# Kernel optimization log

Hardware: AMD Instinct MI355X
Metric: run time of the kernel (lower is better)

## Reference

```python
import jax, jax.numpy as jnp
import numpy as np

N = 8192   # num_nodes
H = 128    # hidden_dim
B = 100    # batch of events
K = 5      # num_neg_samples
TD_MAX = 10000.0
TIME_SD = jnp.array([50.0, 7.0, 15.0, 15.0])  # time_sd from forward; time_mean = 0


def setup_inputs() -> dict:
    key = jax.random.key(0)
    ks = jax.random.split(key, 16)
    p = 32.0 / N  # avg degree ~32
    A = (jax.random.uniform(ks[0], (N, N)) < p).astype(jnp.float32)
    # S init: S[v,u] = 1/D[v] for neighbors u (row-normalized A)
    S = A / (A.sum(axis=1, keepdims=True) + 1e-7)
    z0 = jax.random.normal(ks[1], (N, H)) * 0.1
    u = jax.random.randint(ks[2], (B,), 0, N)
    v = jax.random.randint(ks[3], (B,), 0, N)
    event_types = jax.random.randint(ks[4], (B,), 0, 2)
    neg_idx = jax.random.randint(ks[5], (B, 2 * K), 0, N)
    time_diff = jax.random.normal(ks[6], (B, 2, 4))
    t_bar = jax.random.uniform(ks[7], (B, N)) * 1000.0
    t = 1000.0 + 10.0 * jnp.arange(B, dtype=jnp.float32)

    def lin(k, o, i):
        k1, k2 = jax.random.split(k)
        lim = 1.0 / np.sqrt(i)
        return (jax.random.uniform(k1, (o, i), minval=-lim, maxval=lim),
                jax.random.uniform(k2, (o,), minval=-lim, maxval=lim))

    om0_w, om0_b = lin(ks[8], 1, 2 * H)
    om1_w, om1_b = lin(ks[9], 1, 2 * H)
    Wh_w, Wh_b = lin(ks[10], H, H)
    Ws_w, Ws_b = lin(ks[11], H, H)
    Wr_w, Wr_b = lin(ks[12], H, H)
    Wt_w, Wt_b = lin(ks[13], H, 4)
    return dict(u=u, v=v, event_types=event_types, neg_idx=neg_idx,
                time_diff=time_diff, t_bar=t_bar, t=t, z0=z0, A=A, S=S,
                w_t=0.5 * jnp.ones(2), alpha=0.5 * jnp.ones(2), psi=0.5 * jnp.ones(2),
                om0_w=om0_w, om0_b=om0_b, om1_w=om1_w, om1_b=om1_b,
                Wh_w=Wh_w, Wh_b=Wh_b, Ws_w=Ws_w, Ws_b=Ws_b,
                Wr_w=Wr_w, Wr_b=Wr_b, Wt_w=Wt_w, Wt_b=Wt_b)


def _forward(u, v, event_types, neg_idx, time_diff, t_bar, t, z0, A, S,
             w_t, alpha, psi, om0_w, om0_b, om1_w, om1_b,
             Wh_w, Wh_b, Ws_w, Ws_b, Wr_w, Wr_b, Wt_w, Wt_b):
    td_norm = time_diff / TIME_SD  # (td - 0) / sd

    def hawkes(zu, zv, et, td):
        # lambda = psi * log(1 + exp(g/psi)) + alpha * exp(-w_t * td/td_max)
        zc = jnp.concatenate([zu, zv], axis=-1)
        g0 = jnp.einsum('...d,d->...', zc, om0_w[0]) + om0_b[0]
        g1 = jnp.einsum('...d,d->...', zc, om1_w[0]) + om1_b[0]
        g = jnp.where(et == 0, g0, g1)
        ps, al, wt = psi[et], alpha[et], w_t[et]
        gp = jnp.clip(g / (ps + 1e-7), -75.0, 75.0)
        return ps * jnp.log1p(jnp.exp(gp)) + al * jnp.exp(-wt * (td / TD_MAX))

    ar = jnp.arange(N)

    def step(z, ev):
        u_it, v_it, et, td2, tb, t_it, neg = ev
        z_u, z_v = z[u_it], z[v_it]
        Wh_all = z @ Wh_w.T + Wh_b  # [N,H]

        def struct(node):
            # structural attention over node's neighbors (masked, not dense loop)
            mask = A[node] > 0
            q = jnp.exp(S[node]) * mask
            q = q / (q.sum() + 1e-7)
            hsig = jax.nn.sigmoid(q[:, None] * Wh_all)
            hmax = jnp.where(mask[:, None], hsig, -jnp.inf).max(axis=0)
            return jnp.where(jnp.any(mask), hmax, 0.0)

        # update of u uses struct info from v's neighborhood, and vice versa
        hs = jnp.stack([struct(v_it), struct(u_it)])  # [2,H]
        h = (hs @ Ws_w.T + Ws_b) + (jnp.stack([z_u, z_v]) @ Wr_w.T + Wr_b) + (td2 @ Wt_w.T + Wt_b)
        z_upd = jax.nn.sigmoid(h)
        z_new = z.at[u_it].set(z_upd[0]).at[v_it].set(z_upd[1])

        # negative pairs: (u, v_neg_k) then (u_neg_k, v), using z_prev
        v_neg, u_neg = neg[:K], neg[K:]
        zu_neg = jnp.concatenate([jnp.broadcast_to(z_u, (K, H)), z[u_neg]], 0)
        zv_neg = jnp.concatenate([z[v_neg], jnp.broadcast_to(z_v, (K, H))], 0)
        lt_u = jnp.concatenate([jnp.full((K,), tb[u_it]), tb[u_neg]])
        lt_v = jnp.concatenate([tb[v_neg], jnp.full((K,), tb[v_it])])
        ts_neg = t_it - jnp.maximum(lt_u, lt_v)
        ts_pos = t_it - jnp.maximum(tb[u_it], tb[v_it])

        # all-node intensity prediction (Lambda_dict path, detached in torch)
        zd = jax.lax.stop_gradient(z)
        zu_all = jnp.concatenate([jnp.broadcast_to(jax.lax.stop_gradient(z_u), (N, H)),
                                  jnp.broadcast_to(jax.lax.stop_gradient(z_v), (N, H))], 0)
        zv_all = jnp.concatenate([zd, zd], 0)
        last_t = jnp.maximum(
            jnp.concatenate([jnp.full((N,), tb[u_it]), jnp.full((N,), tb[v_it])]),
            jnp.concatenate([tb, tb]))
        lam_all = hawkes(zu_all, zv_all, jnp.full((2 * N,), et),
                         jax.lax.stop_gradient(t_it - last_t))
        m = ((ar != u_it) & (ar != v_it)).astype(lam_all.dtype)
        lam_sum = jax.lax.stop_gradient(jnp.sum(lam_all * jnp.concatenate([m, m])))

        return z_new, (z_u, z_v, zu_neg, zv_neg, ts_pos, ts_neg, lam_sum)

    _, (zu_p, zv_p, zun, zvn, ts_p, ts_n, lam_sums) = jax.lax.scan(
        step, z0, (u, v, event_types, td_norm, t_bar, t, neg_idx))

    lam_pos = hawkes(zu_p, zv_p, event_types, ts_p)            # [B]
    lam_neg = hawkes(zun, zvn, event_types[:, None], ts_n)      # [B,2K]
    return jnp.concatenate([lam_pos[:, None], lam_neg, lam_sums[:, None]], axis=1)  # [B, 2K+2]


def reference(u, v, event_types, neg_idx, time_diff, t_bar, t, z0, A, S,
              w_t, alpha, psi, om0_w, om0_b, om1_w, om1_b,
              Wh_w, Wh_b, Ws_w, Ws_b, Wr_w, Wr_b, Wt_w, Wt_b):
    return _forward(u, v, event_types, neg_idx, time_diff, t_bar, t, z0, A, S,
                    w_t, alpha, psi, om0_w, om0_b, om1_w, om1_b,
                    Wh_w, Wh_b, Ws_w, Ws_b, Wr_w, Wr_b, Wt_w, Wt_b)
```

## Files before the change

kernel.cpp:

```cpp
#include <hip/hip_runtime.h>
#include <math.h>

#define N 8192
#define H 128
#define BB 100
#define KK 5
#define MAXN 256
#define TD_MAXF 10000.0f

#define OFF_WHALLV ((size_t)N * H)
#define OFF_ZVER (OFF_WHALLV + 2 * BB * H)

__global__ __launch_bounds__(256) void prep_all_kernel(
    const float* __restrict__ Wh, const float* __restrict__ Ws,
    const float* __restrict__ Wr, const float* __restrict__ om0,
    const float* __restrict__ om1, const float* __restrict__ z0,
    float* __restrict__ WhT, float* __restrict__ WsT, float* __restrict__ WrT,
    float* __restrict__ omP, unsigned* __restrict__ flags,
    float* __restrict__ dvec0) {
  const int B0 = H * H, B1 = 2 * H * H, B2 = 3 * H * H;
  const int B3 = B2 + 2 * H, B4 = B2 + 4 * H, B5 = B4 + 4 * BB + 4;
  int idx = blockIdx.x * 256 + threadIdx.x;
  if (idx < B0) {
    int d = idx >> 7, k = idx & (H - 1);
    WhT[k * H + d] = Wh[d * H + k];
  } else if (idx < B1) {
    int e = idx - B0;
    int d = e >> 7, k = e & (H - 1);
    WsT[k * H + d] = Ws[d * H + k];
  } else if (idx < B2) {
    int e = idx - B1;
    int d = e >> 7, k = e & (H - 1);
    WrT[k * H + d] = Wr[d * H + k];
  } else if (idx < B3) {
    int e = idx - B2;
    omP[e] = om0[e];
  } else if (idx < B4) {
    int e = idx - B3;
    omP[2 * H + e] = om1[e];
  } else if (idx < B5) {
    flags[idx - B4] = 0u;
  } else if (idx < B5 + N) {
    int j = idx - B5;
    const float4* zr = (const float4*)(z0 + (size_t)j * H);
    const float4* o0 = (const float4*)om0;
    const float4* o1 = (const float4*)om1;
    float a0 = 0, b0 = 0, a1 = 0, b1 = 0;
    for (int k = 0; k < H / 4; ++k) {
      float4 zv = zr[k];
      float4 l0 = o0[k], r0 = o0[k + H / 4];
      float4 l1 = o1[k], r1 = o1[k + H / 4];
      a0 += zv.x * l0.x + zv.y * l0.y + zv.z * l0.z + zv.w * l0.w;
      b0 += zv.x * r0.x + zv.y * r0.y + zv.z * r0.z + zv.w * r0.w;
      a1 += zv.x * l1.x + zv.y * l1.y + zv.z * l1.z + zv.w * l1.w;
      b1 += zv.x * r1.x + zv.y * r1.y + zv.z * r1.z + zv.w * r1.w;
    }
    dvec0[0 * N + j] = a0;
    dvec0[1 * N + j] = b0;
    dvec0[2 * N + j] = a1;
    dvec0[3 * N + j] = b1;
  }
}

__global__ __launch_bounds__(256) void build_kernel(
    const float* __restrict__ z0, const float* __restrict__ WhT,
    const float* __restrict__ Wh_b, float* __restrict__ whall,
    const int* __restrict__ u_, const int* __restrict__ v_,
    const float* __restrict__ A, const float* __restrict__ S,
    int* __restrict__ cnt, int* __restrict__ nidx, float* __restrict__ nes,
    float* __restrict__ qsum, int* __restrict__ woff, int* __restrict__ zsrc,
    unsigned* __restrict__ need) {
  const int blk = blockIdx.x;
  const int tid = threadIdx.x;
  __shared__ float zr2[2][H];
  __shared__ int cnts[256];
  __shared__ int excl[257];
  __shared__ float ssum[256];
  __shared__ int nidxL[MAXN];
  __shared__ int uL[BB], vL[BB];

  if (blk < N / 2) {
    int r = tid >> 7, d = tid & (H - 1);
    int row = blk * 2 + r;
    zr2[r][d] = z0[(size_t)row * H + d];
    __syncthreads();
    float acc = Wh_b[d];
#pragma unroll 8
    for (int k = 0; k < H; ++k) acc += zr2[r][k] * WhT[k * H + d];
    whall[(size_t)row * H + d] = acc;
    return;
  }

  const int l = blk - N / 2;
  const int b = l >> 1, r = l & 1;
  const int node = r ? u_[b] : v_[b];
  int c = 0;
  float local = 0.0f;
  for (int it = 0; it < N / 256; ++it) {
    int j = it * 256 + tid;
    if (A[(size_t)node * N + j] > 0.0f) {
      ++c;
      local += expf(S[(size_t)node * N + j]);
    }
  }
  cnts[tid] = c;
  ssum[tid] = local;
  __syncthreads();
  if (tid == 0) {
    int s = 0;
    for (int i = 0; i < 256; ++i) { excl[i] = s; s += cnts[i]; }
    excl[256] = s;
  }
  __syncthreads();
  int p = excl[tid];
  for (int it = 0; it < N / 256; ++it) {
    int j = it * 256 + tid;
    if (A[(size_t)node * N + j] > 0.0f) {
      if (p < MAXN) {
        nidx[l * MAXN + p] = j;
        nidxL[p] = j;
        nes[l * MAXN + p] = expf(S[(size_t)node * N + j]);
      }
      ++p;
    }
  }
  if (tid < BB) {
    uL[tid] = u_[tid];
    vL[tid] = v_[tid];
  }
  __syncthreads();
  for (int s = 128; s > 0; s >>= 1) {
    if (tid < s) ssum[tid] += ssum[tid + s];
    __syncthreads();
  }
  const int cM = min(excl[256], MAXN);
  if (tid == 0) {
    cnt[l] = cM;
    qsum[l] = ssum[0];
  }
  for (int i = tid; i < cM; i += 256) {
    int n = nidxL[i];
    int a = -1, row = 0;
    for (int s = b - 1; s >= 0; --s) {
      if (vL[s] == n) { a = s; row = 1; break; }
      if (uL[s] == n) { a = s; row = 0; break; }
    }
    int off;
    if (a < 0) {
      off = n * H;
    } else {
      off = (int)OFF_WHALLV + (2 * a + row) * H;
      atomicOr(&need[b * 4 + (a >> 5)], 1u << (a & 31));
    }
    woff[l * MAXN + i] = off;
  }
  if (r == 0 && tid >= 254) {
    int which = tid - 254;
    int nd = which ? vL[b] : uL[b];
    int a = -1, row = 0;
    for (int s = b - 1; s >= 0; --s) {
      if (vL[s] == nd) { a = s; row = 1; break; }
      if (uL[s] == nd) { a = s; row = 0; break; }
    }
    int sv = -1;
    if (a >= 0) {
      sv = 2 * a + row;
      atomicOr(&need[b * 4 + (a >> 5)], 1u << (a & 31));
    }
    zsrc[2 * b + which] = sv;
  }
}

__global__ __launch_bounds__(1024) void step_kernel(
    const int* __restrict__ u_, const int* __restrict__ v_,
    const float* __restrict__ time_diff, const float* __restrict__ z0,
    const float* __restrict__ WhT, const float* __restrict__ WsT,
    const float* __restrict__ WrT, const float* __restrict__ omP,
    const float* __restrict__ Wh_b, const float* __restrict__ Ws_b,
    const float* __restrict__ Wr_b, const float* __restrict__ Wt_w,
    const float* __restrict__ Wt_b, const float* __restrict__ wsf,
    float* __restrict__ zver, float* __restrict__ whallv,
    float* __restrict__ dlog, const float* __restrict__ qsum_,
    const int* __restrict__ cnt_, const float* __restrict__ nes_,
    const int* __restrict__ woff_, const int* __restrict__ zsrc_,
    const unsigned* __restrict__ need, unsigned* done) {
  const int b = blockIdx.x;
  const int t = threadIdx.x;
  __shared__ float scratch[8][2][H];
  __shared__ float hsS[2][H];
  __shared__ float zrowS[2][H];
  __shared__ float zupdS[2][H];
  __shared__ float td2S[2][4];
  __shared__ int uvS[2];

  const int r = t >> 9;
  const int sub = (t >> 7) & 3;
  const int d = t & (H - 1);
  const int l = 2 * b + r;
  const int c = cnt_[l];
  const float iq = 1.0f / (qsum_[l] + 1e-7f);

  float mx = -INFINITY;
  for (int i = sub; i < c; i += 4) {
    int off = woff_[l * MAXN + i];
    if (off < (int)OFF_WHALLV)
      mx = fmaxf(mx, nes_[l * MAXN + i] * iq * wsf[(size_t)off + d]);
  }
  float zpre = 0.0f;
  int zs = -1;
  if (t < 256) {
    int rr = t >> 7, dd = t & (H - 1);
    zs = zsrc_[2 * b + rr];
    if (zs < 0) {
      int nd = rr ? v_[b] : u_[b];
      zpre = z0[(size_t)nd * H + dd];
    }
  }
  if (t >= 512 && t < 520) {
    int i = t - 512;
    int cc = i & 3;
    float sd = (cc == 0) ? 50.0f : ((cc == 1) ? 7.0f : 15.0f);
    td2S[i >> 2][cc] = time_diff[b * 8 + i] / sd;
  }
  if (t == 0) {
    uvS[0] = u_[b];
    uvS[1] = v_[b];
    for (int w = 0; w < 4; ++w) {
      unsigned nw = need[b * 4 + w];
      if (!nw) continue;
      while ((__hip_atomic_load(&done[w], __ATOMIC_RELAXED,
                                __HIP_MEMORY_SCOPE_AGENT) &
              nw) != nw)
        __builtin_amdgcn_s_sleep(1);
    }
    __threadfence();
  }
  __syncthreads();

  const int ub = uvS[0], vb = uvS[1];

  for (int i = sub; i < c; i += 4) {
    int off = woff_[l * MAXN + i];
    if (off >= (int)OFF_WHALLV)
      mx = fmaxf(mx, nes_[l * MAXN + i] * iq * wsf[(size_t)off + d]);
  }
  scratch[sub][r][d] = mx;
  if (t < 256) {
    int rr = t >> 7, dd = t & (H - 1);
    float zv;
    if (zs < 0)
      zv = zpre;
    else
      zv = wsf[OFF_ZVER + (size_t)zs * H + dd];
    zrowS[rr][dd] = zv;
  }
  __syncthreads();

  if (t < 2 * H) {
    int rr = t >> 7, dd = t & (H - 1);
    float m = fmaxf(fmaxf(scratch[0][rr][dd], scratch[1][rr][dd]),
                    fmaxf(scratch[2][rr][dd], scratch[3][rr][dd]));
    hsS[rr][dd] = (c > 0 || rr != r || true)
                      ? ((cnt_[2 * b + rr] > 0)
                             ? (1.0f / (1.0f + expf(-m)))
                             : 0.0f)
                      : 0.0f;
  }
  __syncthreads();

  {
    int ks = t >> 7;
    int k0 = ks * 16;
    float a0 = 0.0f, a1 = 0.0f;
#pragma unroll 4
    for (int k = k0; k < k0 + 16; ++k) {
      float ws = WsT[k * H + d], wr = WrT[k * H + d];
      a0 += hsS[0][k] * ws + zrowS[0][k] * wr;
      a1 += hsS[1][k] * ws + zrowS[1][k] * wr;
    }
    scratch[ks][0][d] = a0;
    scratch[ks][1][d] = a1;
  }
  __syncthreads();

  if (t < 2 * H) {
    int rr = t >> 7, dd = t & (H - 1);
    float acc = Ws_b[dd] + Wr_b[dd] + Wt_b[dd];
#pragma unroll
    for (int ks = 0; ks < 8; ++ks) acc += scratch[ks][rr][dd];
    acc += td2S[rr][0] * Wt_w[dd * 4 + 0] + td2S[rr][1] * Wt_w[dd * 4 + 1] +
           td2S[rr][2] * Wt_w[dd * 4 + 2] + td2S[rr][3] * Wt_w[dd * 4 + 3];
    float zu = 1.0f / (1.0f + expf(-acc));
    zupdS[rr][dd] = zu;
    zver[(size_t)(2 * b + rr) * H + dd] = zu;
  }
  __syncthreads();

  {
    int ks = t >> 7;
    int k0 = ks * 16;
    int r0 = (ub == vb) ? 1 : 0;
    float a0 = 0.0f, a1 = 0.0f;
#pragma unroll 4
    for (int k = k0; k < k0 + 16; ++k) {
      float wh = WhT[k * H + d];
      a0 += zupdS[r0][k] * wh;
      a1 += zupdS[1][k] * wh;
    }
    scratch[ks][0][d] = a0;
    scratch[ks][1][d] = a1;
  }
  __syncthreads();

  if (t < 2 * H) {
    int rr = t >> 7, dd = t & (H - 1);
    float acc = Wh_b[dd];
#pragma unroll
    for (int ks = 0; ks < 8; ++ks) acc += scratch[ks][rr][dd];
    whallv[(size_t)(2 * b + rr) * H + dd] = acc;
  } else if (t < 768) {
    int w = (t - 256) >> 6;
    int lane = t & 63;
    int row = w >> 2;
    int which = w & 3;
    int rr = (row == 0 && ub == vb) ? 1 : row;
    int wsel = which >> 1;
    int off = (which & 1) * H;
    float val = zupdS[rr][lane] * omP[wsel * 2 * H + off + lane] +
                zupdS[rr][64 + lane] * omP[wsel * 2 * H + off + 64 + lane];
    for (int s = 32; s > 0; s >>= 1) val += __shfl_down(val, s);
    if (lane == 0) dlog[b * 8 + which * 2 + row] = val;
  }
  __syncthreads();

  if (t == 0) {
    __threadfence();
    atomicOr(&done[b >> 5], 1u << (b & 31));
  }
}

__global__ __launch_bounds__(1024) void lam_kernel(
    const int* __restrict__ u, const int* __restrict__ v,
    const int* __restrict__ etypes, const int* __restrict__ neg_,
    const float* __restrict__ t_bar, const float* __restrict__ tt,
    const float* __restrict__ w_t, const float* __restrict__ alpha,
    const float* __restrict__ psi, const float* __restrict__ om0_b,
    const float* __restrict__ om1_b, const float* __restrict__ dvec0,
    const float* __restrict__ dlog, float* __restrict__ out) {
  const int b = blockIdx.x;
  const int tid = threadIdx.x;
  __shared__ float dR[N];
  __shared__ int uS[BB], vS[BB];
  __shared__ float red[1024];
  __shared__ float suS, svS;

  const int e = etypes[b];
  const int ub = u[b], vb = v[b];
  const float ps = psi[e], al = alpha[e], wt = w_t[e];
  const float ob0 = om0_b[0], ob1 = om1_b[0];
  const float ob = e ? ob1 : ob0;
  const float tcur = tt[b];
  const float inv_ps = 1.0f / (ps + 1e-7f);
  const int whichR = 2 * e + 1;
  const int whichL = 2 * e;

  if (tid < BB) {
    uS[tid] = u[tid];
    vS[tid] = v[tid];
  }
  {
    const float4* base = (const float4*)(dvec0 + (size_t)whichR * N);
    float4* dst = (float4*)dR;
    for (int i = tid; i < N / 4; i += 1024) dst[i] = base[i];
  }
  __syncthreads();

  for (int i = tid; i < b; i += 1024) {
    int ui = uS[i], vi = vS[i];
    bool u_over = (ui == vi);
    bool v_over = false;
    for (int j = i + 1; j < b; ++j) {
      int uj = uS[j], vj = vS[j];
      u_over = u_over || (uj == ui) || (vj == ui);
      v_over = v_over || (uj == vi) || (vj == vi);
    }
    if (!u_over) dR[ui] = dlog[i * 8 + whichR * 2 + 0];
    if (!v_over) dR[vi] = dlog[i * 8 + whichR * 2 + 1];
  }

  if (tid < 13) {
    auto dpre = [&](int x, int which) -> float {
      for (int bp = b - 1; bp >= 0; --bp) {
        if (vS[bp] == x) return dlog[bp * 8 + which * 2 + 1];
        if (uS[bp] == x) return dlog[bp * 8 + which * 2 + 0];
      }
      return dvec0[(size_t)which * N + x];
    };
    if (tid < 11) {
      int li, ri;
      float ltu, ltv;
      if (tid == 0) {
        li = ub; ri = vb;
        ltu = t_bar[(size_t)b * N + ub];
        ltv = t_bar[(size_t)b * N + vb];
      } else if (tid <= 5) {
        int vn = neg_[b * (2 * KK) + (tid - 1)];
        li = ub; ri = vn;
        ltu = t_bar[(size_t)b * N + ub];
        ltv = t_bar[(size_t)b * N + vn];
      } else {
        int un = neg_[b * (2 * KK) + (tid - 1)];
        li = un; ri = vb;
        ltu = t_bar[(size_t)b * N + un];
        ltv = t_bar[(size_t)b * N + vb];
      }
      float g = dpre(li, whichL) + dpre(ri, whichR) + ob;
      float gp = fminf(fmaxf(g * inv_ps, -75.0f), 75.0f);
      float ts = tcur - fmaxf(ltu, ltv);
      out[b * 12 + tid] =
          ps * log1pf(expf(gp)) + al * expf(-wt * (ts / TD_MAXF));
    } else if (tid == 11) {
      suS = dpre(ub, whichL);
    } else {
      svS = dpre(vb, whichL);
    }
  }
  __syncthreads();

  const float su = suS, sv = svS;
  const float tb_u = t_bar[(size_t)b * N + ub];
  const float tb_v = t_bar[(size_t)b * N + vb];
  const float4* tb4 = (const float4*)(t_bar + (size_t)b * N);
  const float4* dR4 = (const float4*)dR;
  float acc = 0.0f;
  for (int j4 = tid; j4 < N / 4; j4 += 1024) {
    float4 dv = dR4[j4];
    float4 tb = tb4[j4];
    float de[4] = {dv.x, dv.y, dv.z, dv.w};
    float te[4] = {tb.x, tb.y, tb.z, tb.w};
#pragma unroll
    for (int ee = 0; ee < 4; ++ee) {
      int j = j4 * 4 + ee;
      if (j == ub || j == vb) continue;
      float dd = de[ee];
      float tbj = te[ee];
      float gu = su + dd + ob;
      float gv = sv + dd + ob;
      float gpu_ = fminf(fmaxf(gu * inv_ps, -75.0f), 75.0f);
      float gpv_ = fminf(fmaxf(gv * inv_ps, -75.0f), 75.0f);
      float spl = ps * (log1pf(expf(gpu_)) + log1pf(expf(gpv_)));
      float tdu = tcur - fmaxf(tb_u, tbj);
      float tdv = tcur - fmaxf(tb_v, tbj);
      float ex =
          al * (expf(-wt * (tdu / TD_MAXF)) + expf(-wt * (tdv / TD_MAXF)));
      acc += spl + ex;
    }
  }
  red[tid] = acc;
  __syncthreads();
  for (int s = 512; s > 0; s >>= 1) {
    if (tid < s) red[tid] += red[tid + s];
    __syncthreads();
  }
  if (tid == 0) out[b * 12 + 11] = red[0];
}

extern "C" void kernel_launch(void* const* d_in, const int* in_sizes, int n_in,
                              void* d_out, int out_size, void* d_ws,
                              size_t ws_size, hipStream_t stream) {
  const int* u = (const int*)d_in[0];
  const int* v = (const int*)d_in[1];
  const int* et = (const int*)d_in[2];
  const int* neg = (const int*)d_in[3];
  const float* time_diff = (const float*)d_in[4];
  const float* t_bar = (const float*)d_in[5];
  const float* t = (const float*)d_in[6];
  const float* z0 = (const float*)d_in[7];
  const float* A = (const float*)d_in[8];
  const float* S = (const float*)d_in[9];
  const float* w_t = (const float*)d_in[10];
  const float* alpha = (const float*)d_in[11];
  const float* psi = (const float*)d_in[12];
  const float* om0_w = (const float*)d_in[13];
  const float* om0_b = (const float*)d_in[14];
  const float* om1_w = (const float*)d_in[15];
  const float* om1_b = (const float*)d_in[16];
  const float* Wh_w = (const float*)d_in[17];
  const float* Wh_b = (const float*)d_in[18];
  const float* Ws_w = (const float*)d_in[19];
  const float* Ws_b = (const float*)d_in[20];
  const float* Wr_w = (const float*)d_in[21];
  const float* Wr_b = (const float*)d_in[22];
  const float* Wt_w = (const float*)d_in[23];
  const float* Wt_b = (const float*)d_in[24];
  float* out = (float*)d_out;

  float* wsf = (float*)d_ws;
  float* whall = wsf;
  float* whallv = wsf + OFF_WHALLV;
  float* zver = wsf + OFF_ZVER;
  float* WhT = zver + 2 * BB * H;
  float* WsT = WhT + H * H;
  float* WrT = WsT + H * H;
  float* omP = WrT + H * H;
  float* dvec0 = omP + 4 * H;
  float* dlog = dvec0 + 4 * N;
  float* qsum = dlog + 8 * BB;
  int* cnt = (int*)(qsum + 2 * BB);
  int* nidx = cnt + 2 * BB;
  float* nes = (float*)(nidx + 2 * BB * MAXN);
  int* woff = (int*)(nes + 2 * BB * MAXN);
  int* zsrc = woff + 2 * BB * MAXN;
  unsigned* need = (unsigned*)(zsrc + 2 * BB);
  unsigned* done = need + 4 * BB;

  const int PREP_ELEMS = 3 * H * H + 4 * H + 4 * BB + 4 + N;
  prep_all_kernel<<<(PREP_ELEMS + 255) / 256, 256, 0, stream>>>(
      Wh_w, Ws_w, Wr_w, om0_w, om1_w, z0, WhT, WsT, WrT, omP, need, dvec0);
  build_kernel<<<N / 2 + 2 * BB, 256, 0, stream>>>(
      z0, WhT, Wh_b, whall, u, v, A, S, cnt, nidx, nes, qsum, woff, zsrc,
      need);
  step_kernel<<<BB, 1024, 0, stream>>>(
      u, v, time_diff, z0, WhT, WsT, WrT, omP, Wh_b, Ws_b, Wr_b, Wt_w, Wt_b,
      wsf, zver, whallv, dlog, qsum, cnt, nes, woff, zsrc, need, done);
  lam_kernel<<<BB, 1024, 0, stream>>>(u, v, et, neg, t_bar, t, w_t, alpha, psi,
                                      om0_b, om1_b, dvec0, dlog, out);
}
```

Baseline: 610.3 us.

## Fuse step and lambda kernels into one launch with per-block flag waits

Merges the sequential step kernel and the lambda kernel into a single 200-block launch. The lambda blocks spin on done flags until all earlier steps have finished, so they overlap with the step chain instead of waiting for a kernel boundary. The step blocks also preload their weight columns into registers and stage the neighbour offset and weight lists in shared memory before the dependency wait, taking those loads off the serial critical path. The cost is higher register and shared-memory pressure in every block and a reliance on all 200 blocks being co-resident, since the lambda blocks busy-wait on step blocks.

```diff
diff --git a/kernel.cpp b/kernel.cpp
--- a/kernel.cpp
+++ b/kernel.cpp
@@ -171,191 +171,212 @@
   }
 }
 
-__global__ __launch_bounds__(1024) void step_kernel(
+__global__ __launch_bounds__(1024) void fused_kernel(
     const int* __restrict__ u_, const int* __restrict__ v_,
-    const float* __restrict__ time_diff, const float* __restrict__ z0,
+    const int* __restrict__ et_, const int* __restrict__ neg_,
+    const float* __restrict__ time_diff, const float* __restrict__ t_bar,
+    const float* __restrict__ tt, const float* __restrict__ z0,
     const float* __restrict__ WhT, const float* __restrict__ WsT,
     const float* __restrict__ WrT, const float* __restrict__ omP,
     const float* __restrict__ Wh_b, const float* __restrict__ Ws_b,
     const float* __restrict__ Wr_b, const float* __restrict__ Wt_w,
-    const float* __restrict__ Wt_b, const float* __restrict__ wsf,
-    float* __restrict__ zver, float* __restrict__ whallv,
-    float* __restrict__ dlog, const float* __restrict__ qsum_,
-    const int* __restrict__ cnt_, const float* __restrict__ nes_,
-    const int* __restrict__ woff_, const int* __restrict__ zsrc_,
-    const unsigned* __restrict__ need, unsigned* done) {
-  const int b = blockIdx.x;
+    const float* __restrict__ Wt_b, const float* __restrict__ w_t,
+    const float* __restrict__ alpha, const float* __restrict__ psi,
+    const float* __restrict__ om0_b, const float* __restrict__ om1_b,
+    const float* __restrict__ wsf, float* __restrict__ zver,
+    float* __restrict__ whallv, float* __restrict__ dlog,
+    const float* __restrict__ qsum_, const int* __restrict__ cnt_,
+    const float* __restrict__ nes_, const int* __restrict__ woff_,
+    const int* __restrict__ zsrc_, const float* __restrict__ dvec0,
+    const unsigned* __restrict__ need, unsigned* done,
+    float* __restrict__ out) {
+  const int blk = blockIdx.x;
   const int t = threadIdx.x;
   __shared__ float scratch[8][2][H];
   __shared__ float hsS[2][H];
   __shared__ float zrowS[2][H];
   __shared__ float zupdS[2][H];
   __shared__ float td2S[2][4];
+  __shared__ int woffS[2][MAXN];
+  __shared__ float nqS[2][MAXN];
+  __shared__ int cntS[2];
   __shared__ int uvS[2];
-
-  const int r = t >> 9;
-  const int sub = (t >> 7) & 3;
-  const int d = t & (H - 1);
-  const int l = 2 * b + r;
-  const int c = cnt_[l];
-  const float iq = 1.0f / (qsum_[l] + 1e-7f);
-
-  float mx = -INFINITY;
-  for (int i = sub; i < c; i += 4) {
-    int off = woff_[l * MAXN + i];
-    if (off < (int)OFF_WHALLV)
-      mx = fmaxf(mx, nes_[l * MAXN + i] * iq * wsf[(size_t)off + d]);
-  }
-  float zpre = 0.0f;
-  int zs = -1;
-  if (t < 256) {
-    int rr = t >> 7, dd = t & (H - 1);
-    zs = zsrc_[2 * b + rr];
-    if (zs < 0) {
-      int nd = rr ? v_[b] : u_[b];
-      zpre = z0[(size_t)nd * H + dd];
-    }
-  }
-  if (t >= 512 && t < 520) {
-    int i = t - 512;
-    int cc = i & 3;
-    float sd = (cc == 0) ? 50.0f : ((cc == 1) ? 7.0f : 15.0f);
-    td2S[i >> 2][cc] = time_diff[b * 8 + i] / sd;
-  }
-  if (t == 0) {
-    uvS[0] = u_[b];
-    uvS[1] = v_[b];
-    for (int w = 0; w < 4; ++w) {
-      unsigned nw = need[b * 4 + w];
-      if (!nw) continue;
-      while ((__hip_atomic_load(&done[w], __ATOMIC_RELAXED,
-                                __HIP_MEMORY_SCOPE_AGENT) &
-              nw) != nw)
-        __builtin_amdgcn_s_sleep(1);
-    }
-    __threadfence();
-  }
-  __syncthreads();
-
-  const int ub = uvS[0], vb = uvS[1];
-
-  for (int i = sub; i < c; i += 4) {
-    int off = woff_[l * MAXN + i];
-    if (off >= (int)OFF_WHALLV)
-      mx = fmaxf(mx, nes_[l * MAXN + i] * iq * wsf[(size_t)off + d]);
-  }
-  scratch[sub][r][d] = mx;
-  if (t < 256) {
-    int rr = t >> 7, dd = t & (H - 1);
-    float zv;
-    if (zs < 0)
-      zv = zpre;
-    else
-      zv = wsf[OFF_ZVER + (size_t)zs * H + dd];
-    zrowS[rr][dd] = zv;
-  }
-  __syncthreads();
-
-  if (t < 2 * H) {
-    int rr = t >> 7, dd = t & (H - 1);
-    float m = fmaxf(fmaxf(scratch[0][rr][dd], scratch[1][rr][dd]),
-                    fmaxf(scratch[2][rr][dd], scratch[3][rr][dd]));
-    hsS[rr][dd] = (c > 0 || rr != r || true)
-                      ? ((cnt_[2 * b + rr] > 0)
-                             ? (1.0f / (1.0f + expf(-m)))
-                             : 0.0f)
-                      : 0.0f;
-  }
-  __syncthreads();
-
-  {
-    int ks = t >> 7;
-    int k0 = ks * 16;
-    float a0 = 0.0f, a1 = 0.0f;
-#pragma unroll 4
-    for (int k = k0; k < k0 + 16; ++k) {
-      float ws = WsT[k * H + d], wr = WrT[k * H + d];
-      a0 += hsS[0][k] * ws + zrowS[0][k] * wr;
-      a1 += hsS[1][k] * ws + zrowS[1][k] * wr;
-    }
-    scratch[ks][0][d] = a0;
-    scratch[ks][1][d] = a1;
-  }
-  __syncthreads();
-
-  if (t < 2 * H) {
-    int rr = t >> 7, dd = t & (H - 1);
-    float acc = Ws_b[dd] + Wr_b[dd] + Wt_b[dd];
-#pragma unroll
-    for (int ks = 0; ks < 8; ++ks) acc += scratch[ks][rr][dd];
-    acc += td2S[rr][0] * Wt_w[dd * 4 + 0] + td2S[rr][1] * Wt_w[dd * 4 + 1] +
-           td2S[rr][2] * Wt_w[dd * 4 + 2] + td2S[rr][3] * Wt_w[dd * 4 + 3];
-    float zu = 1.0f / (1.0f + expf(-acc));
-    zupdS[rr][dd] = zu;
-    zver[(size_t)(2 * b + rr) * H + dd] = zu;
-  }
-  __syncthreads();
-
-  {
-    int ks = t >> 7;
-    int k0 = ks * 16;
-    int r0 = (ub == vb) ? 1 : 0;
-    float a0 = 0.0f, a1 = 0.0f;
-#pragma unroll 4
-    for (int k = k0; k < k0 + 16; ++k) {
-      float wh = WhT[k * H + d];
-      a0 += zupdS[r0][k] * wh;
-      a1 += zupdS[1][k] * wh;
-    }
-    scratch[ks][0][d] = a0;
-    scratch[ks][1][d] = a1;
-  }
-  __syncthreads();
-
-  if (t < 2 * H) {
-    int rr = t >> 7, dd = t & (H - 1);
-    float acc = Wh_b[dd];
-#pragma unroll
-    for (int ks = 0; ks < 8; ++ks) acc += scratch[ks][rr][dd];
-    whallv[(size_t)(2 * b + rr) * H + dd] = acc;
-  } else if (t < 768) {
-    int w = (t - 256) >> 6;
-    int lane = t & 63;
-    int row = w >> 2;
-    int which = w & 3;
-    int rr = (row == 0 && ub == vb) ? 1 : row;
-    int wsel = which >> 1;
-    int off = (which & 1) * H;
-    float val = zupdS[rr][lane] * omP[wsel * 2 * H + off + lane] +
-                zupdS[rr][64 + lane] * omP[wsel * 2 * H + off + 64 + lane];
-    for (int s = 32; s > 0; s >>= 1) val += __shfl_down(val, s);
-    if (lane == 0) dlog[b * 8 + which * 2 + row] = val;
-  }
-  __syncthreads();
-
-  if (t == 0) {
-    __threadfence();
-    atomicOr(&done[b >> 5], 1u << (b & 31));
-  }
-}
-
-__global__ __launch_bounds__(1024) void lam_kernel(
-    const int* __restrict__ u, const int* __restrict__ v,
-    const int* __restrict__ etypes, const int* __restrict__ neg_,
-    const float* __restrict__ t_bar, const float* __restrict__ tt,
-    const float* __restrict__ w_t, const float* __restrict__ alpha,
-    const float* __restrict__ psi, const float* __restrict__ om0_b,
-    const float* __restrict__ om1_b, const float* __restrict__ dvec0,
-    const float* __restrict__ dlog, float* __restrict__ out) {
-  const int b = blockIdx.x;
-  const int tid = threadIdx.x;
   __shared__ float dR[N];
   __shared__ int uS[BB], vS[BB];
   __shared__ float red[1024];
   __shared__ float suS, svS;
 
-  const int e = etypes[b];
-  const int ub = u[b], vb = v[b];
+  if (blk < BB) {
+    const int b = blk;
+    const int r = t >> 9;
+    const int sub = (t >> 7) & 3;
+    const int d = t & (H - 1);
+    const int l = 2 * b + r;
+    const int c = cnt_[l];
+    const float iq = 1.0f / (qsum_[l] + 1e-7f);
+    const int ks = t >> 7;
+    const int k0 = ks * 16;
+
+    if (t < 512) {
+      int rr = t >> 8, i = t & 255;
+      woffS[rr][i] = woff_[(2 * b + rr) * MAXN + i];
+      nqS[rr][i] = nes_[(2 * b + rr) * MAXN + i];
+    } else if (t < 520) {
+      int i = t - 512;
+      int cc = i & 3;
+      float sd = (cc == 0) ? 50.0f : ((cc == 1) ? 7.0f : 15.0f);
+      td2S[i >> 2][cc] = time_diff[b * 8 + i] / sd;
+    } else if (t < 522) {
+      cntS[t - 520] = cnt_[2 * b + (t - 520)];
+    } else if (t == 522) {
+      uvS[0] = u_[b];
+    } else if (t == 523) {
+      uvS[1] = v_[b];
+    }
+    float wsReg[16], wrReg[16], whReg[16];
+#pragma unroll
+    for (int kk = 0; kk < 16; ++kk) {
+      wsReg[kk] = WsT[(k0 + kk) * H + d];
+      wrReg[kk] = WrT[(k0 + kk) * H + d];
+      whReg[kk] = WhT[(k0 + kk) * H + d];
+    }
+    float biasReg = 0.0f, whbReg = 0.0f;
+    float4 wt4Reg = {0.0f, 0.0f, 0.0f, 0.0f};
+    float zpre = 0.0f;
+    int zs = -1;
+    if (t < 256) {
+      int dd = t & (H - 1);
+      biasReg = Ws_b[dd] + Wr_b[dd] + Wt_b[dd];
+      whbReg = Wh_b[dd];
+      wt4Reg = ((const float4*)Wt_w)[dd];
+      int rr = t >> 7;
+      zs = zsrc_[2 * b + rr];
+      if (zs < 0) {
+        int nd = rr ? v_[b] : u_[b];
+        zpre = z0[(size_t)nd * H + dd];
+      }
+    }
+    float omA = 0.0f, omB = 0.0f;
+    if (t >= 256 && t < 768) {
+      int w = (t - 256) >> 6;
+      int lane = t & 63;
+      int which = w & 3;
+      int wsel = which >> 1;
+      int offo = (which & 1) * H;
+      omA = omP[wsel * 2 * H + offo + lane];
+      omB = omP[wsel * 2 * H + offo + 64 + lane];
+    }
+    __syncthreads();
+
+    float mx = -INFINITY;
+    for (int i = sub; i < c; i += 4) {
+      int off = woffS[r][i];
+      if (off < (int)OFF_WHALLV)
+        mx = fmaxf(mx, nqS[r][i] * iq * wsf[(size_t)off + d]);
+    }
+    if (t == 0) {
+      for (int w = 0; w < 4; ++w) {
+        unsigned nw = need[b * 4 + w];
+        if (!nw) continue;
+        while ((__hip_atomic_load(&done[w], __ATOMIC_RELAXED,
+                                  __HIP_MEMORY_SCOPE_AGENT) &
+                nw) != nw)
+          __builtin_amdgcn_s_sleep(1);
+      }
+      __threadfence();
+    }
+    __syncthreads();
+
+    const int ub = uvS[0], vb = uvS[1];
+
+    for (int i = sub; i < c; i += 4) {
+      int off = woffS[r][i];
+      if (off >= (int)OFF_WHALLV)
+        mx = fmaxf(mx, nqS[r][i] * iq * wsf[(size_t)off + d]);
+    }
+    scratch[sub][r][d] = mx;
+    if (t < 256) {
+      int rr = t >> 7, dd = t & (H - 1);
+      zrowS[rr][dd] = (zs < 0) ? zpre : wsf[OFF_ZVER + (size_t)zs * H + dd];
+    }
+    __syncthreads();
+
+    if (t < 2 * H) {
+      int rr = t >> 7, dd = t & (H - 1);
+      float m = fmaxf(fmaxf(scratch[0][rr][dd], scratch[1][rr][dd]),
+                      fmaxf(scratch[2][rr][dd], scratch[3][rr][dd]));
+      hsS[rr][dd] = (cntS[rr] > 0) ? (1.0f / (1.0f + expf(-m))) : 0.0f;
+    }
+    __syncthreads();
+
+    {
+      float a0 = 0.0f, a1 = 0.0f;
+#pragma unroll
+      for (int kk = 0; kk < 16; ++kk) {
+        int k = k0 + kk;
+        a0 += hsS[0][k] * wsReg[kk] + zrowS[0][k] * wrReg[kk];
+        a1 += hsS[1][k] * wsReg[kk] + zrowS[1][k] * wrReg[kk];
+      }
+      scratch[ks][0][d] = a0;
+      scratch[ks][1][d] = a1;
+    }
+    __syncthreads();
+
+    if (t < 2 * H) {
+      int rr = t >> 7, dd = t & (H - 1);
+      float acc = biasReg;
+#pragma unroll
+      for (int kx = 0; kx < 8; ++kx) acc += scratch[kx][rr][dd];
+      acc += td2S[rr][0] * wt4Reg.x + td2S[rr][1] * wt4Reg.y +
+             td2S[rr][2] * wt4Reg.z + td2S[rr][3] * wt4Reg.w;
+      float zu = 1.0f / (1.0f + expf(-acc));
+      zupdS[rr][dd] = zu;
+      zver[(size_t)(2 * b + rr) * H + dd] = zu;
+    }
+    __syncthreads();
+
+    {
+      int r0 = (ub == vb) ? 1 : 0;
+      float f0 = 0.0f, f1 = 0.0f;
+#pragma unroll
+      for (int kk = 0; kk < 16; ++kk) {
+        int k = k0 + kk;
+        f0 += zupdS[r0][k] * whReg[kk];
+        f1 += zupdS[1][k] * whReg[kk];
+      }
+      scratch[ks][0][d] = f0;
+      scratch[ks][1][d] = f1;
+    }
+    __syncthreads();
+
+    if (t < 2 * H) {
+      int rr = t >> 7, dd = t & (H - 1);
+      float acc = whbReg;
+#pragma unroll
+      for (int kx = 0; kx < 8; ++kx) acc += scratch[kx][rr][dd];
+      whallv[(size_t)(2 * b + rr) * H + dd] = acc;
+    } else if (t < 768) {
+      int w = (t - 256) >> 6;
+      int lane = t & 63;
+      int row = w >> 2;
+      int which = w & 3;
+      int rr = (row == 0 && ub == vb) ? 1 : row;
+      float val = zupdS[rr][lane] * omA + zupdS[rr][64 + lane] * omB;
+      for (int s = 32; s > 0; s >>= 1) val += __shfl_down(val, s);
+      if (lane == 0) dlog[b * 8 + which * 2 + row] = val;
+    }
+    __syncthreads();
+
+    if (t == 0) {
+      __threadfence();
+      atomicOr(&done[b >> 5], 1u << (b & 31));
+    }
+    return;
+  }
+
+  const int b = blk - BB;
+  const int e = et_[b];
+  const int ub = u_[b], vb = v_[b];
   const float ps = psi[e], al = alpha[e], wt = w_t[e];
   const float ob0 = om0_b[0], ob1 = om1_b[0];
   const float ob = e ? ob1 : ob0;
@@ -364,18 +385,31 @@
   const int whichR = 2 * e + 1;
   const int whichL = 2 * e;
 
-  if (tid < BB) {
-    uS[tid] = u[tid];
-    vS[tid] = v[tid];
+  if (t < BB) {
+    uS[t] = u_[t];
+    vS[t] = v_[t];
   }
   {
     const float4* base = (const float4*)(dvec0 + (size_t)whichR * N);
     float4* dst = (float4*)dR;
-    for (int i = tid; i < N / 4; i += 1024) dst[i] = base[i];
+    for (int i = t; i < N / 4; i += 1024) dst[i] = base[i];
+  }
+  if (t == 0) {
+    for (int w = 0; w < 4; ++w) {
+      int cb = b - 32 * w;
+      unsigned nw =
+          (cb >= 32) ? 0xffffffffu : (cb <= 0 ? 0u : ((1u << cb) - 1u));
+      if (!nw) continue;
+      while ((__hip_atomic_load(&done[w], __ATOMIC_RELAXED,
+                                __HIP_MEMORY_SCOPE_AGENT) &
+              nw) != nw)
+        __builtin_amdgcn_s_sleep(1);
+    }
+    __threadfence();
   }
   __syncthreads();
 
-  for (int i = tid; i < b; i += 1024) {
+  for (int i = t; i < b; i += 1024) {
     int ui = uS[i], vi = vS[i];
     bool u_over = (ui == vi);
     bool v_over = false;
@@ -388,7 +422,7 @@
     if (!v_over) dR[vi] = dlog[i * 8 + whichR * 2 + 1];
   }
 
-  if (tid < 13) {
+  if (t < 13) {
     auto dpre = [&](int x, int which) -> float {
       for (int bp = b - 1; bp >= 0; --bp) {
         if (vS[bp] == x) return dlog[bp * 8 + which * 2 + 1];
@@ -396,20 +430,20 @@
       }
       return dvec0[(size_t)which * N + x];
     };
-    if (tid < 11) {
+    if (t < 11) {
       int li, ri;
       float ltu, ltv;
-      if (tid == 0) {
+      if (t == 0) {
         li = ub; ri = vb;
         ltu = t_bar[(size_t)b * N + ub];
         ltv = t_bar[(size_t)b * N + vb];
-      } else if (tid <= 5) {
-        int vn = neg_[b * (2 * KK) + (tid - 1)];
+      } else if (t <= 5) {
+        int vn = neg_[b * (2 * KK) + (t - 1)];
         li = ub; ri = vn;
         ltu = t_bar[(size_t)b * N + ub];
         ltv = t_bar[(size_t)b * N + vn];
       } else {
-        int un = neg_[b * (2 * KK) + (tid - 1)];
+        int un = neg_[b * (2 * KK) + (t - 1)];
         li = un; ri = vb;
         ltu = t_bar[(size_t)b * N + un];
         ltv = t_bar[(size_t)b * N + vb];
@@ -417,9 +451,8 @@
       float g = dpre(li, whichL) + dpre(ri, whichR) + ob;
       float gp = fminf(fmaxf(g * inv_ps, -75.0f), 75.0f);
       float ts = tcur - fmaxf(ltu, ltv);
-      out[b * 12 + tid] =
-          ps * log1pf(expf(gp)) + al * expf(-wt * (ts / TD_MAXF));
-    } else if (tid == 11) {
+      out[b * 12 + t] = ps * log1pf(expf(gp)) + al * expf(-wt * (ts / TD_MAXF));
+    } else if (t == 11) {
       suS = dpre(ub, whichL);
     } else {
       svS = dpre(vb, whichL);
@@ -433,7 +466,7 @@
   const float4* tb4 = (const float4*)(t_bar + (size_t)b * N);
   const float4* dR4 = (const float4*)dR;
   float acc = 0.0f;
-  for (int j4 = tid; j4 < N / 4; j4 += 1024) {
+  for (int j4 = t; j4 < N / 4; j4 += 1024) {
     float4 dv = dR4[j4];
     float4 tb = tb4[j4];
     float de[4] = {dv.x, dv.y, dv.z, dv.w};
@@ -456,13 +489,13 @@
       acc += spl + ex;
     }
   }
-  red[tid] = acc;
+  red[t] = acc;
   __syncthreads();
   for (int s = 512; s > 0; s >>= 1) {
-    if (tid < s) red[tid] += red[tid + s];
-    __syncthreads();
-  }
-  if (tid == 0) out[b * 12 + 11] = red[0];
+    if (t < s) red[t] += red[t + s];
+    __syncthreads();
+  }
+  if (t == 0) out[b * 12 + 11] = red[0];
 }
 
 extern "C" void kernel_launch(void* const* d_in, const int* in_sizes, int n_in,
@@ -520,9 +553,8 @@
   build_kernel<<<N / 2 + 2 * BB, 256, 0, stream>>>(
       z0, WhT, Wh_b, whall, u, v, A, S, cnt, nidx, nes, qsum, woff, zsrc,
       need);
-  step_kernel<<<BB, 1024, 0, stream>>>(
-      u, v, time_diff, z0, WhT, WsT, WrT, omP, Wh_b, Ws_b, Wr_b, Wt_w, Wt_b,
-      wsf, zver, whallv, dlog, qsum, cnt, nes, woff, zsrc, need, done);
-  lam_kernel<<<BB, 1024, 0, stream>>>(u, v, et, neg, t_bar, t, w_t, alpha, psi,
-                                      om0_b, om1_b, dvec0, dlog, out);
+  fused_kernel<<<2 * BB, 1024, 0, stream>>>(
+      u, v, et, neg, time_diff, t_bar, t, z0, WhT, WsT, WrT, omP, Wh_b, Ws_b,
+      Wr_b, Wt_w, Wt_b, w_t, alpha, psi, om0_b, om1_b, wsf, zver, whallv,
+      dlog, qsum, cnt, nes, woff, zsrc, dvec0, need, done, out);
 }
```

Measured after the change: 606.1 us. About the same (-0.7%).
